# Kernel optimization log

Measured on AMD Instinct MI355X. Metric: run time of the kernel, lower is better.

## Reference

```python
import jax, jax.numpy as jnp
import numpy as np

TEMPERATURE = 0.1
EPS = 1e-08
NEG_INF = -9e15


def setup_inputs() -> dict:
    key = jax.random.key(0)
    k1, k2 = jax.random.split(key)
    B, D = 4096, 256
    z_i = jax.random.normal(k1, (B, D), dtype=jnp.float32)
    z_j = jax.random.normal(k2, (B, D), dtype=jnp.float32)
    mask_positive = jnp.ones((B,), dtype=bool)
    return {"z_i": z_i, "z_j": z_j, "mask_positive": mask_positive}


def reference(z_i, z_j, mask_positive):
    B = z_i.shape[0]
    N = 2 * B
    z = jnp.concatenate([z_i, z_j], axis=0)  # [N, D]
    # cosine similarity: normalize (norms clamped to eps) then GEMM
    norms = jnp.maximum(jnp.linalg.norm(z, axis=1, keepdims=True), EPS)
    zn = z / norms
    sim = jnp.matmul(zn, zn.T) / TEMPERATURE  # [N, N]
    # mask self-similarity on diagonal
    rows = jnp.arange(N)
    sim = sim.at[rows, rows].set(NEG_INF)
    logprob = jax.nn.log_softmax(sim, axis=1)
    # positive of row k is row (k+B) mod N
    positives = jnp.concatenate([jnp.arange(B, N), jnp.arange(0, B)])
    loss_vec = -logprob[rows, positives]  # [N]
    mp = jnp.concatenate([mask_positive, mask_positive])  # [N] bool
    cnt = jnp.sum(mp.astype(jnp.float32))
    total = jnp.sum(jnp.where(mp, loss_vec, 0.0))
    loss = jnp.where(cnt > 0, total / jnp.maximum(cnt, 1.0), 0.0)
    return loss
```

## Files before the change

kernel.cpp:

```cpp
#include <hip/hip_runtime.h>
#include <hip/hip_bf16.h>

#define NTOT   8192
#define BHALF  4096
#define DDIM   256
#define SMOD   16
#define NPART  4
#define MAXSLOT 9
#define EXPSCALE 14.4269504088896341f

typedef __attribute__((ext_vector_type(8))) short bf16x8_t;
typedef __attribute__((ext_vector_type(4))) float f32x4_t;

__device__ inline unsigned short f2bf(float x) {
    __hip_bfloat16 h = __float2bfloat16(x);
    return __builtin_bit_cast(unsigned short, h);
}

__global__ void norm_pair_kernel(const float* __restrict__ zi,
                                 const float* __restrict__ zj,
                                 unsigned short* __restrict__ zn,
                                 float* __restrict__ posdot,
                                 float* __restrict__ s_part) {
    int gtid = blockIdx.x * 256 + threadIdx.x;
    if (gtid < NTOT * NPART) s_part[gtid] = 0.0f;
    int k    = gtid >> 6;
    int lane = gtid & 63;
    float4 vi = reinterpret_cast<const float4*>(zi + (size_t)k * DDIM)[lane];
    float4 vj = reinterpret_cast<const float4*>(zj + (size_t)k * DDIM)[lane];
    float ssi = vi.x*vi.x + vi.y*vi.y + vi.z*vi.z + vi.w*vi.w;
    float ssj = vj.x*vj.x + vj.y*vj.y + vj.z*vj.z + vj.w*vj.w;
    float dot = vi.x*vj.x + vi.y*vj.y + vi.z*vj.z + vi.w*vj.w;
    #pragma unroll
    for (int off = 32; off >= 1; off >>= 1) {
        ssi += __shfl_xor(ssi, off);
        ssj += __shfl_xor(ssj, off);
        dot += __shfl_xor(dot, off);
    }
    float ri = 1.0f / fmaxf(sqrtf(ssi), 1e-8f);
    float rj = 1.0f / fmaxf(sqrtf(ssj), 1e-8f);
    ushort4 oi, oj;
    oi.x = f2bf(vi.x * ri); oi.y = f2bf(vi.y * ri);
    oi.z = f2bf(vi.z * ri); oi.w = f2bf(vi.w * ri);
    oj.x = f2bf(vj.x * rj); oj.y = f2bf(vj.y * rj);
    oj.z = f2bf(vj.z * rj); oj.w = f2bf(vj.w * rj);
    reinterpret_cast<ushort4*>(zn + (size_t)k * DDIM)[lane] = oi;
    reinterpret_cast<ushort4*>(zn + (size_t)(k + BHALF) * DDIM)[lane] = oj;
    if (lane == 0) posdot[k] = dot * ri * rj * 10.0f;
}

__global__ void __launch_bounds__(256, 2)
gemm_sym_kernel(const unsigned short* __restrict__ zn,
                float* __restrict__ s_part) {
    __shared__ unsigned short ldsB[2][64 * 256];
    __shared__ float colLDS[MAXSLOT][4][64];

    const int tid  = threadIdx.x;
    const int lane = tid & 63;
    const int wv   = tid >> 6;
    const int m    = lane & 15;
    const int quad = lane >> 4;
    const int biA  = blockIdx.x;
    const int s    = blockIdx.y;

    float* rowPart = s_part + (size_t)(s   & (NPART - 1)) * NTOT;
    float* colPart = s_part + (size_t)(biA & (NPART - 1)) * NTOT;

    const int sr = tid >> 5;
    const int sc = tid & 31;

    int slot = 0;
    #pragma unroll
    for (int p = 0; p < 2; ++p) {
        const int bi = p ? (63 - biA) : biA;
        const int R0 = bi << 7;
        const int cs0 = 2 * bi + ((s - 2 * bi) & (SMOD - 1));
        if (cs0 >= 128) continue;

        bf16x8_t afrag[2][8];
        #pragma unroll
        for (int rf = 0; rf < 2; ++rf) {
            const unsigned short* arow = zn + (size_t)(R0 + wv*32 + rf*16 + m) * DDIM;
            #pragma unroll
            for (int kk = 0; kk < 8; ++kk)
                afrag[rf][kk] = *reinterpret_cast<const bf16x8_t*>(arow + kk*32 + quad*8);
        }

        float rowacc[2][4] = {{0.f,0.f,0.f,0.f},{0.f,0.f,0.f,0.f}};

        {
            const int C0 = cs0 << 6;
            #pragma unroll
            for (int t = 0; t < 8; ++t) {
                const int r = t * 8 + sr;
                const unsigned short* g =
                    zn + (size_t)(C0 + r) * DDIM + ((sc ^ (r & 7)) << 3);
                __builtin_amdgcn_global_load_lds(
                    (const __attribute__((address_space(1))) unsigned int*)g,
                    (__attribute__((address_space(3))) unsigned int*)
                        &ldsB[0][(t * 256 + tid) * 8],
                    16, 0, 0);
            }
        }

        int cur = 0;
        for (int cs = cs0; cs < 128; cs += SMOD) {
            const int C0 = cs << 6;
            const bool isDiag = ((cs >> 1) == bi);

            asm volatile("s_waitcnt vmcnt(0)" ::: "memory");
            __builtin_amdgcn_s_barrier();
            __builtin_amdgcn_sched_barrier(0);

            if (cs + SMOD < 128) {
                const int C1 = (cs + SMOD) << 6;
                unsigned short* dst = ldsB[cur ^ 1];
                #pragma unroll
                for (int t = 0; t < 8; ++t) {
                    const int r = t * 8 + sr;
                    const unsigned short* g =
                        zn + (size_t)(C1 + r) * DDIM + ((sc ^ (r & 7)) << 3);
                    __builtin_amdgcn_global_load_lds(
                        (const __attribute__((address_space(1))) unsigned int*)g,
                        (__attribute__((address_space(3))) unsigned int*)
                            (dst + (t * 256 + tid) * 8),
                        16, 0, 0);
                }
            }

            const unsigned short* Bt = ldsB[cur];
            #pragma unroll
            for (int cf = 0; cf < 4; ++cf) {
                f32x4_t c0 = (f32x4_t){0.f,0.f,0.f,0.f};
                f32x4_t c1 = (f32x4_t){0.f,0.f,0.f,0.f};
                #pragma unroll
                for (int kk = 0; kk < 8; ++kk) {
                    bf16x8_t b = *reinterpret_cast<const bf16x8_t*>(
                        Bt + (cf*16 + m) * 256 + (((kk*4 + quad) ^ (m & 7)) << 3));
                    c0 = __builtin_amdgcn_mfma_f32_16x16x32_bf16(afrag[0][kk], b, c0, 0, 0, 0);
                    c1 = __builtin_amdgcn_mfma_f32_16x16x32_bf16(afrag[1][kk], b, c1, 0, 0, 0);
                }
                const int gc = C0 + cf*16 + m;
                float colsum = 0.f;
                #pragma unroll
                for (int r = 0; r < 4; ++r) {
                    int gr0 = R0 + wv*32 + quad*4 + r;
                    float e0 = exp2f(c0[r] * EXPSCALE);
                    float e1 = exp2f(c1[r] * EXPSCALE);
                    if (isDiag && gr0 == gc)        e0 = 0.f;
                    if (isDiag && (gr0 + 16) == gc) e1 = 0.f;
                    rowacc[0][r] += e0;
                    rowacc[1][r] += e1;
                    colsum += e0 + e1;
                }
                if (!isDiag) {
                    colsum += __shfl_xor(colsum, 16);
                    colsum += __shfl_xor(colsum, 32);
                    if (quad == 0) colLDS[slot][wv][cf*16 + m] = colsum;
                }
            }
            cur ^= 1;
            ++slot;
        }

        #pragma unroll
        for (int rf = 0; rf < 2; ++rf)
            #pragma unroll
            for (int r = 0; r < 4; ++r) {
                float v = rowacc[rf][r];
                v += __shfl_xor(v, 1);
                v += __shfl_xor(v, 2);
                v += __shfl_xor(v, 4);
                v += __shfl_xor(v, 8);
                if (m == 0)
                    atomicAdd(&rowPart[R0 + wv*32 + rf*16 + quad*4 + r], v);
            }

        __builtin_amdgcn_s_barrier();
        __builtin_amdgcn_sched_barrier(0);
    }

    asm volatile("s_waitcnt lgkmcnt(0)" ::: "memory");
    __builtin_amdgcn_s_barrier();
    __builtin_amdgcn_sched_barrier(0);

    if (tid < 64) {
        int slot2 = 0;
        #pragma unroll
        for (int p = 0; p < 2; ++p) {
            const int bi = p ? (63 - biA) : biA;
            const int cs0 = 2 * bi + ((s - 2 * bi) & (SMOD - 1));
            if (cs0 >= 128) continue;
            for (int cs = cs0; cs < 128; cs += SMOD) {
                if ((cs >> 1) != bi) {
                    float v = colLDS[slot2][0][tid] + colLDS[slot2][1][tid]
                            + colLDS[slot2][2][tid] + colLDS[slot2][3][tid];
                    atomicAdd(&colPart[(cs << 6) + tid], v);
                }
                ++slot2;
            }
        }
    }
}

__global__ void finalize_kernel(const float* __restrict__ s_part,
                                const float* __restrict__ posdot,
                                const unsigned char* __restrict__ mask,
                                float* __restrict__ out) {
    int tid = threadIdx.x, lane = tid & 63, wv = tid >> 6;
    float tot = 0.f, cnt = 0.f;
    #pragma unroll
    for (int si = 0; si < NTOT / 1024; ++si) {
        int k = si * 1024 + tid;
        int kb = k & (BHALF - 1);
        if (mask[kb] != 0) {
            float sk = s_part[k] + s_part[NTOT + k]
                     + s_part[2*NTOT + k] + s_part[3*NTOT + k];
            tot += __logf(sk) - posdot[kb];
            cnt += 1.f;
        }
    }
    #pragma unroll
    for (int off = 32; off >= 1; off >>= 1) {
        tot += __shfl_xor(tot, off);
        cnt += __shfl_xor(cnt, off);
    }
    __shared__ float st[16], sc[16];
    if (lane == 0) { st[wv] = tot; sc[wv] = cnt; }
    __syncthreads();
    if (tid == 0) {
        float T = 0.f, C = 0.f;
        #pragma unroll
        for (int i = 0; i < 16; ++i) { T += st[i]; C += sc[i]; }
        out[0] = (C > 0.f) ? (T / fmaxf(C, 1.f)) : 0.f;
    }
}

extern "C" void kernel_launch(void* const* d_in, const int* in_sizes, int n_in,
                              void* d_out, int out_size, void* d_ws, size_t ws_size,
                              hipStream_t stream) {
    const float* zi = (const float*)d_in[0];
    const float* zj = (const float*)d_in[1];
    const unsigned char* mask = (const unsigned char*)d_in[2];
    float* out = (float*)d_out;

    unsigned short* zn = (unsigned short*)d_ws;
    float* s_part = (float*)((char*)d_ws + (size_t)NTOT * DDIM * 2);
    float* posdot = s_part + NPART * NTOT;

    norm_pair_kernel<<<dim3(1024), dim3(256), 0, stream>>>(zi, zj, zn, posdot, s_part);
    gemm_sym_kernel<<<dim3(32, SMOD), dim3(256), 0, stream>>>(zn, s_part);
    finalize_kernel<<<dim3(1), dim3(1024), 0, stream>>>(s_part, posdot, mask, out);
}
```

Baseline: 105.7 us.

## Double GEMM block to 512 threads, splitting column strips across wave halves

The symmetric GEMM block grows from 4 to 8 waves. The two halves of waves each compute half of the 64-column strip per step, so each wave runs 2 column fragments instead of 4. Global-to-LDS staging is spread over the larger thread count through a new helper. The aim is more waves in flight per CU to hide latency, at the cost of each half loading the same A fragments into registers. It also adds more atomics for row partials, and the 512x4 launch bound may force a tighter register limit that causes spills.

Measured after the change: 110.4 us. 1.04x slower.

```diff
diff --git a/kernel.cpp b/kernel.cpp
--- a/kernel.cpp
+++ b/kernel.cpp
@@ -49,7 +49,23 @@
     if (lane == 0) posdot[k] = dot * ri * rj * 10.0f;
 }
 
-__global__ void __launch_bounds__(256, 2)
+__device__ __forceinline__ void stage_strip(const unsigned short* __restrict__ zn,
+                                            int C0, unsigned short* dst,
+                                            int tid, int sc, int sr7) {
+    #pragma unroll
+    for (int t = 0; t < 4; ++t) {
+        const int ci = t * 512 + tid;
+        const int r  = ci >> 5;
+        const unsigned short* g =
+            zn + (size_t)(C0 + r) * DDIM + ((sc ^ sr7) << 3);
+        __builtin_amdgcn_global_load_lds(
+            (const __attribute__((address_space(1))) unsigned int*)g,
+            (__attribute__((address_space(3))) unsigned int*)(dst + (size_t)ci * 8),
+            16, 0, 0);
+    }
+}
+
+__global__ void __launch_bounds__(512, 4)
 gemm_sym_kernel(const unsigned short* __restrict__ zn,
                 float* __restrict__ s_part) {
     __shared__ unsigned short ldsB[2][64 * 256];
@@ -57,7 +73,9 @@
 
     const int tid  = threadIdx.x;
     const int lane = tid & 63;
-    const int wv   = tid >> 6;
+    const int w    = tid >> 6;
+    const int wv   = w & 3;
+    const int h    = w >> 2;
     const int m    = lane & 15;
     const int quad = lane >> 4;
     const int biA  = blockIdx.x;
@@ -66,8 +84,8 @@
     float* rowPart = s_part + (size_t)(s   & (NPART - 1)) * NTOT;
     float* colPart = s_part + (size_t)(biA & (NPART - 1)) * NTOT;
 
-    const int sr = tid >> 5;
-    const int sc = tid & 31;
+    const int sr7 = (tid >> 5) & 7;
+    const int sc  = tid & 31;
 
     int slot = 0;
     #pragma unroll
@@ -88,20 +106,7 @@
 
         float rowacc[2][4] = {{0.f,0.f,0.f,0.f},{0.f,0.f,0.f,0.f}};
 
-        {
-            const int C0 = cs0 << 6;
-            #pragma unroll
-            for (int t = 0; t < 8; ++t) {
-                const int r = t * 8 + sr;
-                const unsigned short* g =
-                    zn + (size_t)(C0 + r) * DDIM + ((sc ^ (r & 7)) << 3);
-                __builtin_amdgcn_global_load_lds(
-                    (const __attribute__((address_space(1))) unsigned int*)g,
-                    (__attribute__((address_space(3))) unsigned int*)
-                        &ldsB[0][(t * 256 + tid) * 8],
-                    16, 0, 0);
-            }
-        }
+        stage_strip(zn, cs0 << 6, ldsB[0], tid, sc, sr7);
 
         int cur = 0;
         for (int cs = cs0; cs < 128; cs += SMOD) {
@@ -112,35 +117,23 @@
             __builtin_amdgcn_s_barrier();
             __builtin_amdgcn_sched_barrier(0);
 
-            if (cs + SMOD < 128) {
-                const int C1 = (cs + SMOD) << 6;
-                unsigned short* dst = ldsB[cur ^ 1];
-                #pragma unroll
-                for (int t = 0; t < 8; ++t) {
-                    const int r = t * 8 + sr;
-                    const unsigned short* g =
-                        zn + (size_t)(C1 + r) * DDIM + ((sc ^ (r & 7)) << 3);
-                    __builtin_amdgcn_global_load_lds(
-                        (const __attribute__((address_space(1))) unsigned int*)g,
-                        (__attribute__((address_space(3))) unsigned int*)
-                            (dst + (t * 256 + tid) * 8),
-                        16, 0, 0);
-                }
-            }
+            if (cs + SMOD < 128)
+                stage_strip(zn, (cs + SMOD) << 6, ldsB[cur ^ 1], tid, sc, sr7);
 
             const unsigned short* Bt = ldsB[cur];
             #pragma unroll
-            for (int cf = 0; cf < 4; ++cf) {
+            for (int cfl = 0; cfl < 2; ++cfl) {
+                const int colbase = h * 32 + cfl * 16;
                 f32x4_t c0 = (f32x4_t){0.f,0.f,0.f,0.f};
                 f32x4_t c1 = (f32x4_t){0.f,0.f,0.f,0.f};
                 #pragma unroll
                 for (int kk = 0; kk < 8; ++kk) {
                     bf16x8_t b = *reinterpret_cast<const bf16x8_t*>(
-                        Bt + (cf*16 + m) * 256 + (((kk*4 + quad) ^ (m & 7)) << 3));
+                        Bt + (colbase + m) * 256 + (((kk*4 + quad) ^ (m & 7)) << 3));
                     c0 = __builtin_amdgcn_mfma_f32_16x16x32_bf16(afrag[0][kk], b, c0, 0, 0, 0);
                     c1 = __builtin_amdgcn_mfma_f32_16x16x32_bf16(afrag[1][kk], b, c1, 0, 0, 0);
                 }
-                const int gc = C0 + cf*16 + m;
+                const int gc = C0 + colbase + m;
                 float colsum = 0.f;
                 #pragma unroll
                 for (int r = 0; r < 4; ++r) {
@@ -156,7 +149,7 @@
                 if (!isDiag) {
                     colsum += __shfl_xor(colsum, 16);
                     colsum += __shfl_xor(colsum, 32);
-                    if (quad == 0) colLDS[slot][wv][cf*16 + m] = colsum;
+                    if (quad == 0) colLDS[slot][wv][colbase + m] = colsum;
                 }
             }
             cur ^= 1;
@@ -249,6 +242,6 @@
     float* posdot = s_part + NPART * NTOT;
 
     norm_pair_kernel<<<dim3(1024), dim3(256), 0, stream>>>(zi, zj, zn, posdot, s_part);
-    gemm_sym_kernel<<<dim3(32, SMOD), dim3(256), 0, stream>>>(zn, s_part);
+    gemm_sym_kernel<<<dim3(32, SMOD), dim3(512), 0, stream>>>(zn, s_part);
     finalize_kernel<<<dim3(1), dim3(1024), 0, stream>>>(s_part, posdot, mask, out);
 }
```
